# Kernel optimization log

Hardware: AMD Instinct MI355X
Metric: run time of the kernel (lower is better)

The kernel has to match this reference:

```python
import jax, jax.numpy as jnp
import numpy as np

N, E, FS = 50000, 400000, 256
H, D = 8, 64            # GAT heads, hidden_size (per-head out_feats)
NH, DK, DV = 8, 64, 64  # transformer MHA
B = 1024
NEG_SLOPE = 0.2
EPS = 1e-6


def _layer_norm(x, g, b, eps=EPS):
    mu = x.mean(-1, keepdims=True)
    var = x.var(-1, keepdims=True)
    return (x - mu) / jnp.sqrt(var + eps) * g + b


def setup_inputs() -> dict:
    key = jax.random.key(0)
    ks = jax.random.split(key, 20)
    s = 0.02
    return {
        "features": jax.random.normal(ks[0], (N, FS), jnp.float32),
        "src": jax.random.randint(ks[1], (E,), 0, N, jnp.int32),
        "dst": jax.random.randint(ks[2], (E,), 0, N, jnp.int32),
        "url": jax.random.randint(ks[3], (B,), 1, N + 1, jnp.int32),  # 1-based ids
        # GATConv params (DGL-style)
        "gat_fc_w": jax.random.normal(ks[4], (FS, H * D), jnp.float32) * s,
        "attn_l": jax.random.normal(ks[5], (H, D), jnp.float32) * s,
        "attn_r": jax.random.normal(ks[6], (H, D), jnp.float32) * s,
        "gat_res_w": jax.random.normal(ks[7], (FS, H * D), jnp.float32) * s,
        "gat_bias": jnp.zeros((H, D), jnp.float32),
        # post-GAT LayerNorm
        "ln_g": jnp.ones((D,), jnp.float32),
        "ln_b": jnp.zeros((D,), jnp.float32),
        # MultiHeadAttention params
        "wq": jax.random.normal(ks[8], (D, NH * DK), jnp.float32) * s,
        "wk": jax.random.normal(ks[9], (D, NH * DK), jnp.float32) * s,
        "wv": jax.random.normal(ks[10], (D, NH * DV), jnp.float32) * s,
        "fc_w": jax.random.normal(ks[11], (NH * DV, D), jnp.float32) * s,
        "fc_b": jnp.zeros((D,), jnp.float32),
        "mha_ln_g": jnp.ones((D,), jnp.float32),
        "mha_ln_b": jnp.zeros((D,), jnp.float32),
        # final classifier
        "out_w": jax.random.normal(ks[12], (D, 2), jnp.float32) * s,
        "out_b": jnp.zeros((2,), jnp.float32),
    }


def reference(features, src, dst, url, gat_fc_w, attn_l, attn_r, gat_res_w,
              gat_bias, ln_g, ln_b, wq, wk, wv, fc_w, fc_b, mha_ln_g,
              mha_ln_b, out_w, out_b):
    # ---- GATConv (residual=True, bias, negative_slope=0.2, no activation) ----
    feat = (features @ gat_fc_w).reshape(N, H, D)          # [N,H,D]
    el = jnp.einsum('nhd,hd->nh', feat, attn_l)            # [N,H]
    er = jnp.einsum('nhd,hd->nh', feat, attn_r)            # [N,H]
    e = jax.nn.leaky_relu(el[src] + er[dst], NEG_SLOPE)    # [E,H] edge scores
    # segment softmax over incoming edges of each dst node
    m = jax.ops.segment_max(e, dst, num_segments=N)        # [N,H]
    m = jnp.where(jnp.isfinite(m), m, 0.0)
    ex = jnp.exp(e - m[dst])                               # [E,H]
    denom = jax.ops.segment_sum(ex, dst, num_segments=N)   # [N,H]
    a = ex / jnp.maximum(denom[dst], 1e-20)                # [E,H]
    msg = feat[src] * a[:, :, None]                        # [E,H,D]
    rst = jax.ops.segment_sum(msg, dst, num_segments=N)    # [N,H,D]
    res = (features @ gat_res_w).reshape(N, H, D)
    gat_emb = rst + res + gat_bias                         # [N,H,D]

    # ---- select batch nodes (url is 1-based) ----
    ids = url - 1
    x = gat_emb[ids]                                       # [B,H,D]
    x = _layer_norm(x, ln_g, ln_b)

    # ---- dense multi-head self-attention over the H gat heads (seq dim) ----
    residual = x
    q = (x @ wq).reshape(B, H, NH, DK)
    k = (x @ wk).reshape(B, H, NH, DK)
    v = (x @ wv).reshape(B, H, NH, DV)
    attn = jnp.einsum('bqhd,bkhd->bhqk', q, k) / jnp.sqrt(jnp.float32(DK))
    attn = jax.nn.softmax(attn, axis=-1)
    o = jnp.einsum('bhqk,bkhd->bqhd', attn, v).reshape(B, H, NH * DV)
    o = o @ fc_w + fc_b                                    # [B,H,D]
    o = _layer_norm(o + residual, mha_ln_g, mha_ln_b)

    # ---- pool + classify ----
    pooled = o.sum(axis=1)                                 # [B,D]
    logits = pooled @ out_w + out_b                        # [B,2]
    return logits
```

## Files before the change

### kernel.cpp

```cpp
#include <hip/hip_runtime.h>
#include <math.h>

#define Nn 50000
#define Ee 400000
#define FSz 256
#define HD_ 512
#define Bb 1024

static __device__ __forceinline__ int clampi(int v, int lo, int hi){
    return v < lo ? lo : (v > hi ? hi : v);
}
static __device__ __forceinline__ unsigned short f2bf(float f){
    unsigned int u = __float_as_uint(f);
    unsigned int r = u + 0x7FFFu + ((u >> 16) & 1u);
    return (unsigned short)(r >> 16);
}
static __device__ __forceinline__ float bflo(unsigned int v){ return __uint_as_float(v << 16); }
static __device__ __forceinline__ float bfhi(unsigned int v){ return __uint_as_float(v & 0xFFFF0000u); }

__global__ __launch_bounds__(256) void k_mark(const int* __restrict__ url, int* uid, int* unode, int* cnt,
                                              const float* __restrict__ W,
                                              const float* __restrict__ al,
                                              const float* __restrict__ ar,
                                              float* __restrict__ wl, float* __restrict__ wr){
    int t = threadIdx.x;
    if(blockIdx.x >= 4){
        int bi = blockIdx.x - 4;
        int wv = t >> 6, lane = t & 63;
        #pragma unroll
        for(int r = 0; r < 4; r++){
            int f = bi*16 + wv*4 + r;
            float pl[8], pr[8];
            #pragma unroll
            for(int h = 0; h < 8; h++){
                float w = W[f*512 + h*64 + lane];
                pl[h] = w * al[h*64 + lane];
                pr[h] = w * ar[h*64 + lane];
            }
            #pragma unroll
            for(int h = 0; h < 8; h++){
                #pragma unroll
                for(int m = 32; m >= 1; m >>= 1){
                    pl[h] += __shfl_xor(pl[h], m, 64);
                    pr[h] += __shfl_xor(pr[h], m, 64);
                }
            }
            #pragma unroll
            for(int h = 0; h < 8; h++){
                if(lane == h){ wl[h*256 + f] = pl[h]; wr[h*256 + f] = pr[h]; }
            }
        }
    } else {
        int b = blockIdx.x * 256 + t;
        if(b < Bb){
            int n = clampi(url[b] - 1, 0, Nn - 1);
            int old = atomicCAS(&uid[n], -1, -2);
            if(old == -1){
                int id = atomicAdd(cnt, 1);
                unode[id] = n;
                uid[n] = id;
            }
        }
    }
}

__global__ __launch_bounds__(256) void k_scatter(const int* __restrict__ src, const int* __restrict__ dst,
                                                 const int* __restrict__ uid, int* __restrict__ fill,
                                                 int* __restrict__ slist){
    int e = blockIdx.x * 256 + threadIdx.x;
    if(e >= Ee) return;
    int d = dst[e];
    if((unsigned)d >= (unsigned)Nn) return;
    int u = uid[d];
    if(u < 0) return;
    int pos = atomicAdd(&fill[u], 1);
    if(pos >= 64) return;
    slist[u*64 + pos] = clampi(src[e], 0, Nn - 1);
}

__global__ __launch_bounds__(256) void k_gat(const float* __restrict__ features,
                                             const float* __restrict__ Wfc,
                                             const float* __restrict__ Wres,
                                             const float* __restrict__ bias,
                                             const float* __restrict__ wl,
                                             const float* __restrict__ wr,
                                             const int* __restrict__ cnt, const int* __restrict__ unode,
                                             const int* __restrict__ fill, const int* __restrict__ slist,
                                             float* __restrict__ gemb){
    int t = threadIdx.x;
    int lane = t & 63, wv = t >> 6;
    int cntv = cnt[0];
    int u0 = blockIdx.x * 4;
    if(u0 >= cntv) return;

    __shared__ float cxs[4][8][256];
    __shared__ float fres[4][256];
    __shared__ float sew[4][64][8];
    __shared__ float ser[4][8];
    __shared__ int   sslist[4][64];

    for(int i = t; i < 4*64*8; i += 256) ((float*)sew)[i] = 0.f;

    float4 rwl[8], rwr[8];
    #pragma unroll
    for(int h = 0; h < 8; h++){
        rwl[h] = *(const float4*)&wl[h*256 + 4*lane];
        rwr[h] = *(const float4*)&wr[h*256 + 4*lane];
    }

    int dg[4];
    #pragma unroll
    for(int j = 0; j < 4; j++){
        int u = u0 + j;
        dg[j] = (u < cntv) ? min(fill[u], 64) : 0;
        if(t < dg[j]) sslist[j][t] = slist[u*64 + t];
        if(u < cntv) fres[j][t] = features[(size_t)unode[u] * FSz + t];
        else         fres[j][t] = 0.f;
    }
    __syncthreads();

    int c1 = dg[0], c2 = c1 + dg[1], c3 = c2 + dg[2];
    int total = c3 + dg[3];
    for(int tau = wv; tau < total + 4; tau += 4){
        int j, i, isEr = 0;
        if(tau < c1){ j = 0; i = tau; }
        else if(tau < c2){ j = 1; i = tau - c1; }
        else if(tau < c3){ j = 2; i = tau - c2; }
        else if(tau < total){ j = 3; i = tau - c3; }
        else { j = tau - total; i = 0; isEr = 1; }
        int s = isEr ? ((u0 + j < cntv) ? unode[u0 + j] : 0) : sslist[j][i];
        float4 x = *(const float4*)(features + (size_t)s * FSz + 4*lane);
        float p[8];
        if(isEr){
            #pragma unroll
            for(int h = 0; h < 8; h++)
                p[h] = x.x*rwr[h].x + x.y*rwr[h].y + x.z*rwr[h].z + x.w*rwr[h].w;
        } else {
            #pragma unroll
            for(int h = 0; h < 8; h++)
                p[h] = x.x*rwl[h].x + x.y*rwl[h].y + x.z*rwl[h].z + x.w*rwl[h].w;
        }
        #pragma unroll
        for(int h = 0; h < 8; h++){
            #pragma unroll
            for(int m = 32; m >= 1; m >>= 1) p[h] += __shfl_xor(p[h], m, 64);
        }
        if(lane == 0){
            if(isEr){
                #pragma unroll
                for(int h = 0; h < 8; h++) ser[j][h] = p[h];
            } else {
                #pragma unroll
                for(int h = 0; h < 8; h++) sew[j][i][h] = p[h];
            }
        }
    }
    __syncthreads();
    if(t < 32){
        int j = t >> 3, h = t & 7;
        int dgj = dg[j];
        if(dgj > 0){
            float ern = ser[j][h];
            float m = -1e30f;
            for(int i = 0; i < dgj; i++){
                float v = sew[j][i][h] + ern;
                v = v > 0.f ? v : 0.2f * v;
                m = fmaxf(m, v);
            }
            float sum = 0.f;
            for(int i = 0; i < dgj; i++){
                float v = sew[j][i][h] + ern;
                v = v > 0.f ? v : 0.2f * v;
                float w = expf(v - m);
                sum += w;
                sew[j][i][h] = w;
            }
            float inv = 1.0f / fmaxf(sum, 1e-20f);
            for(int i = 0; i < dgj; i++) sew[j][i][h] *= inv;
        }
    }
    __syncthreads();
    {
        float cx[4][8];
        #pragma unroll
        for(int j = 0; j < 4; j++)
            #pragma unroll
            for(int h = 0; h < 8; h++) cx[j][h] = 0.f;
        int mxd = max(max(dg[0], dg[1]), max(dg[2], dg[3]));
        for(int i = 0; i < mxd; i++){
            float x[4];
            #pragma unroll
            for(int j = 0; j < 4; j++){
                int s = (i < dg[j]) ? sslist[j][i] : 0;
                x[j] = features[(size_t)s * FSz + t];
            }
            #pragma unroll
            for(int j = 0; j < 4; j++){
                const float* av = &sew[j][i][0];
                float xm = (i < dg[j]) ? x[j] : 0.f;
                #pragma unroll
                for(int h = 0; h < 8; h++) cx[j][h] += av[h] * xm;
            }
        }
        #pragma unroll
        for(int j = 0; j < 4; j++)
            #pragma unroll
            for(int h = 0; h < 8; h++) cxs[j][h][t] = cx[j][h];
    }
    __syncthreads();

    int h = t >> 5;
    int o0 = 2 * t;
    const float2* Wfc2  = (const float2*)Wfc;
    const float2* Wres2 = (const float2*)Wres;
    float a[4][2] = {{0,0},{0,0},{0,0},{0,0}};
    for(int f = 0; f < 256; f += 4){
        float2 w0 = Wfc2[(f+0)*256 + t];
        float2 w1 = Wfc2[(f+1)*256 + t];
        float2 w2 = Wfc2[(f+2)*256 + t];
        float2 w3 = Wfc2[(f+3)*256 + t];
        float2 r0 = Wres2[(f+0)*256 + t];
        float2 r1 = Wres2[(f+1)*256 + t];
        float2 r2 = Wres2[(f+2)*256 + t];
        float2 r3 = Wres2[(f+3)*256 + t];
        #pragma unroll
        for(int j = 0; j < 4; j++){
            float4 c = *(const float4*)&cxs[j][h][f];
            float4 x = *(const float4*)&fres[j][f];
            a[j][0] += c.x*w0.x + c.y*w1.x + c.z*w2.x + c.w*w3.x
                     + x.x*r0.x + x.y*r1.x + x.z*r2.x + x.w*r3.x;
            a[j][1] += c.x*w0.y + c.y*w1.y + c.z*w2.y + c.w*w3.y
                     + x.x*r0.y + x.y*r1.y + x.z*r2.y + x.w*r3.y;
        }
    }
    float b0 = bias[o0], b1 = bias[o0 + 1];
    #pragma unroll
    for(int j = 0; j < 4; j++){
        if(u0 + j < cntv){
            float2* gp = (float2*)(gemb + (size_t)(u0 + j) * HD_);
            gp[t] = make_float2(a[j][0] + b0, a[j][1] + b1);
        }
    }
}

__global__ __launch_bounds__(256, 4) void k_mha(const int* __restrict__ url, const int* __restrict__ uid,
                                             const float* __restrict__ gemb,
                                             const float* __restrict__ lng, const float* __restrict__ lnb,
                                             const float* __restrict__ wq, const float* __restrict__ wk,
                                             const float* __restrict__ wvp, const float* __restrict__ fcw,
                                             const float* __restrict__ fcb, const float* __restrict__ mlg,
                                             const float* __restrict__ mlb, const float* __restrict__ outw,
                                             const float* __restrict__ outb, float* __restrict__ out){
    __shared__ float A[512];
    __shared__ float xnF[512];
    __shared__ unsigned short xnT[64*8];
    __shared__ unsigned short qkb[2*8*520];
    __shared__ float mu8[8], rs8[8], pooled[64];

    int b = blockIdx.x, t = threadIdx.x;
    int lane = t & 63, wv = t >> 6;
    int n = clampi(url[b] - 1, 0, Nn - 1);
    int u = uid[n];
    if(u < 0) u = 0;
    const float* gp = gemb + (size_t)u * HD_;
    A[t] = gp[t]; A[t + 256] = gp[t + 256];
    __syncthreads();
    if(t < 8){
        float s = 0.f, s2 = 0.f;
        for(int d = 0; d < 64; d++){ float v = A[t*64 + d]; s += v; s2 += v * v; }
        float mu = s * (1.0f/64.0f);
        float var = s2 * (1.0f/64.0f) - mu * mu;
        mu8[t] = mu; rs8[t] = rsqrtf(fmaxf(var, 0.0f) + 1e-6f);
    }
    __syncthreads();
    #pragma unroll
    for(int p = 0; p < 2; p++){
        int i = p*256 + t; int q = i >> 6, d = i & 63;
        float xv = (A[i] - mu8[q]) * rs8[q] * lng[d] + lnb[d];
        xnF[i] = xv;
        xnT[d*8 + q] = f2bf(xv);
    }
    __syncthreads();
    float aq0[8] = {0,0,0,0,0,0,0,0}, aq1[8] = {0,0,0,0,0,0,0,0};
    float ak0[8] = {0,0,0,0,0,0,0,0}, ak1[8] = {0,0,0,0,0,0,0,0};
    float av0[8] = {0,0,0,0,0,0,0,0}, av1[8] = {0,0,0,0,0,0,0,0};
    #pragma unroll 2
    for(int d = 0; d < 64; d++){
        float q0 = wq[d*512 + t],  q1 = wq[d*512 + t + 256];
        float k0 = wk[d*512 + t],  k1 = wk[d*512 + t + 256];
        float v0 = wvp[d*512 + t], v1 = wvp[d*512 + t + 256];
        uint4 xp = *(const uint4*)&xnT[d*8];
        float xv[8] = { bflo(xp.x), bfhi(xp.x), bflo(xp.y), bfhi(xp.y),
                        bflo(xp.z), bfhi(xp.z), bflo(xp.w), bfhi(xp.w) };
        #pragma unroll
        for(int r = 0; r < 8; r++){
            aq0[r] += xv[r]*q0; aq1[r] += xv[r]*q1;
            ak0[r] += xv[r]*k0; ak1[r] += xv[r]*k1;
            av0[r] += xv[r]*v0; av1[r] += xv[r]*v1;
        }
    }
    #pragma unroll
    for(int qq = 0; qq < 8; qq++){
        qkb[qq*520 + t]              = f2bf(aq0[qq]);
        qkb[qq*520 + t + 256]        = f2bf(aq1[qq]);
        qkb[4160 + qq*520 + t]       = f2bf(ak0[qq]);
        qkb[4160 + qq*520 + t + 256] = f2bf(ak1[qq]);
    }
    __syncthreads();
    #pragma unroll
    for(int p = 0; p < 2; p++){
        int idx = p*256 + t;
        int nh = idx >> 6, qq = (idx >> 3) & 7, kk = idx & 7;
        const unsigned short* qrow = &qkb[qq*520 + nh*64];
        const unsigned short* krow = &qkb[4160 + kk*520 + nh*64];
        float s = 0.f;
        #pragma unroll
        for(int d8 = 0; d8 < 64; d8 += 8){
            uint4 qv = *(const uint4*)&qrow[d8];
            uint4 kv = *(const uint4*)&krow[d8];
            s += bflo(qv.x)*bflo(kv.x) + bfhi(qv.x)*bfhi(kv.x)
               + bflo(qv.y)*bflo(kv.y) + bfhi(qv.y)*bfhi(kv.y)
               + bflo(qv.z)*bflo(kv.z) + bfhi(qv.z)*bfhi(kv.z)
               + bflo(qv.w)*bflo(kv.w) + bfhi(qv.w)*bfhi(kv.w);
        }
        A[idx] = s * 0.125f;
    }
    __syncthreads();
    if(t < 64){
        float mx = -1e30f;
        #pragma unroll
        for(int k = 0; k < 8; k++) mx = fmaxf(mx, A[t*8 + k]);
        float e[8]; float s = 0.f;
        #pragma unroll
        for(int k = 0; k < 8; k++){ e[k] = expf(A[t*8 + k] - mx); s += e[k]; }
        float inv = 1.0f / s;
        #pragma unroll
        for(int k = 0; k < 8; k++) A[t*8 + k] = e[k] * inv;
    }
    __syncthreads();
    {
        int nh0 = wv;
        #pragma unroll
        for(int qq = 0; qq < 8; qq++){
            const float* s0 = &A[nh0*64 + qq*8];
            const float* s1 = &A[(nh0+4)*64 + qq*8];
            float4 a0 = *(const float4*)s0, b0 = *(const float4*)(s0 + 4);
            float4 a1 = *(const float4*)s1, b1 = *(const float4*)(s1 + 4);
            float o0 = a0.x*av0[0] + a0.y*av0[1] + a0.z*av0[2] + a0.w*av0[3]
                     + b0.x*av0[4] + b0.y*av0[5] + b0.z*av0[6] + b0.w*av0[7];
            float o1 = a1.x*av1[0] + a1.y*av1[1] + a1.z*av1[2] + a1.w*av1[3]
                     + b1.x*av1[4] + b1.y*av1[5] + b1.z*av1[6] + b1.w*av1[7];
            qkb[qq*520 + t]       = f2bf(o0);
            qkb[qq*520 + t + 256] = f2bf(o1);
        }
    }
    __syncthreads();
    {
        float* P = (float*)&qkb[4160];
        int g = lane & 31;
        int qh = lane >> 5;
        int k0 = wv * 128;
        float a[4][2] = {{0,0},{0,0},{0,0},{0,0}};
        const float2* fw2 = (const float2*)fcw;
        for(int k = k0; k < k0 + 128; k += 8){
            float2 f0 = fw2[(k+0)*32 + g];
            float2 f1 = fw2[(k+1)*32 + g];
            float2 f2 = fw2[(k+2)*32 + g];
            float2 f3 = fw2[(k+3)*32 + g];
            float2 f4 = fw2[(k+4)*32 + g];
            float2 f5 = fw2[(k+5)*32 + g];
            float2 f6 = fw2[(k+6)*32 + g];
            float2 f7 = fw2[(k+7)*32 + g];
            #pragma unroll
            for(int jq = 0; jq < 4; jq++){
                int qq = qh*4 + jq;
                uint4 op = *(const uint4*)&qkb[qq*520 + k];
                float x0 = bflo(op.x), x1 = bfhi(op.x), x2 = bflo(op.y), x3 = bfhi(op.y);
                float x4 = bflo(op.z), x5 = bfhi(op.z), x6 = bflo(op.w), x7 = bfhi(op.w);
                a[jq][0] += x0*f0.x + x1*f1.x + x2*f2.x + x3*f3.x + x4*f4.x + x5*f5.x + x6*f6.x + x7*f7.x;
                a[jq][1] += x0*f0.y + x1*f1.y + x2*f2.y + x3*f3.y + x4*f4.y + x5*f5.y + x6*f6.y + x7*f7.y;
            }
        }
        __syncthreads();
        #pragma unroll
        for(int jq = 0; jq < 4; jq++){
            int qq = qh*4 + jq;
            *(float2*)&P[wv*512 + qq*64 + 2*g] = make_float2(a[jq][0], a[jq][1]);
        }
        __syncthreads();
        #pragma unroll
        for(int p = 0; p < 2; p++){
            int o = p*256 + t;
            int dd = o & 63;
            A[o] = P[o] + P[512 + o] + P[1024 + o] + P[1536 + o] + fcb[dd] + xnF[o];
        }
    }
    __syncthreads();
    if(t < 8){
        float s = 0.f, s2 = 0.f;
        for(int d = 0; d < 64; d++){ float v = A[t*64 + d]; s += v; s2 += v * v; }
        float mu = s * (1.0f/64.0f);
        float var = s2 * (1.0f/64.0f) - mu * mu;
        mu8[t] = mu; rs8[t] = rsqrtf(fmaxf(var, 0.0f) + 1e-6f);
    }
    __syncthreads();
    if(t < 64){
        float g2 = mlg[t], bb = mlb[t];
        float s = 0.f;
        #pragma unroll
        for(int qq = 0; qq < 8; qq++)
            s += (A[qq*64 + t] - mu8[qq]) * rs8[qq] * g2 + bb;
        pooled[t] = s;
    }
    __syncthreads();
    if(t < 2){
        float s = outb[t];
        for(int d = 0; d < 64; d++) s += pooled[d] * outw[d*2 + t];
        out[b*2 + t] = s;
    }
}

extern "C" void kernel_launch(void* const* d_in, const int* in_sizes, int n_in,
                              void* d_out, int out_size, void* d_ws, size_t ws_size,
                              hipStream_t stream){
    (void)in_sizes; (void)n_in; (void)out_size; (void)ws_size;
    const float* features  = (const float*)d_in[0];
    const int*   src       = (const int*)d_in[1];
    const int*   dst       = (const int*)d_in[2];
    const int*   url       = (const int*)d_in[3];
    const float* gat_fc_w  = (const float*)d_in[4];
    const float* attn_l    = (const float*)d_in[5];
    const float* attn_r    = (const float*)d_in[6];
    const float* gat_res_w = (const float*)d_in[7];
    const float* gat_bias  = (const float*)d_in[8];
    const float* ln_g      = (const float*)d_in[9];
    const float* ln_b      = (const float*)d_in[10];
    const float* wq        = (const float*)d_in[11];
    const float* wk        = (const float*)d_in[12];
    const float* wv        = (const float*)d_in[13];
    const float* fc_w      = (const float*)d_in[14];
    const float* fc_b      = (const float*)d_in[15];
    const float* mha_ln_g  = (const float*)d_in[16];
    const float* mha_ln_b  = (const float*)d_in[17];
    const float* out_w     = (const float*)d_in[18];
    const float* out_b     = (const float*)d_in[19];

    char* base = (char*)d_ws;
    size_t cur = 0;
    auto alloc = [&](size_t nbytes) -> void* {
        void* p = base + cur;
        cur = (cur + nbytes + 255) & ~(size_t)255;
        return p;
    };
    float* wl    = (float*)alloc(2048 * sizeof(float));
    float* wr    = (float*)alloc(2048 * sizeof(float));
    int*   uid   = (int*)alloc((size_t)Nn * sizeof(int));
    int*   unode = (int*)alloc(1024 * sizeof(int));
    int*   fill  = (int*)alloc(1056 * sizeof(int));
    int*   cnt   = fill + 1024;
    int*   slist = (int*)alloc((size_t)1024 * 64 * sizeof(int));
    float* gemb  = (float*)alloc((size_t)1024 * 512 * sizeof(float));

    hipMemsetAsync(uid, 0xFF, (size_t)Nn * sizeof(int), stream);
    hipMemsetAsync(fill, 0, 1056 * sizeof(int), stream);

    hipLaunchKernelGGL(k_mark,    dim3(20),   dim3(256), 0, stream, url, uid, unode, cnt,
                       gat_fc_w, attn_l, attn_r, wl, wr);
    hipLaunchKernelGGL(k_scatter, dim3(1563), dim3(256), 0, stream, src, dst, uid, fill, slist);
    hipLaunchKernelGGL(k_gat,     dim3(256),  dim3(256), 0, stream, features, gat_fc_w, gat_res_w, gat_bias,
                       wl, wr, cnt, unode, fill, slist, gemb);
    hipLaunchKernelGGL(k_mha,     dim3(1024), dim3(256), 0, stream, url, uid, gemb, ln_g, ln_b,
                       wq, wk, wv, fc_w, fc_b, mha_ln_g, mha_ln_b, out_w, out_b,
                       (float*)d_out);
}
```

Measured before the change: 220.9 us.

## Replace global node-id map with per-block shared hash; batch two samples per MHA block

The scatter kernel now builds a per-block shared-memory hash table from url to batch indices and scatters each edge to every batch entry that shares the destination node. This removes the 50K-entry uid memset, the separate mark kernel and the dedup step. The GAT kernel now processes all 1024 batch entries directly, duplicates included, so it does redundant work when url repeats. The MHA kernel handles two batch rows per block, reusing each weight load across both, at the cost of more registers and occupancy lowered from 4 to 2.

```diff
diff --git a/kernel.cpp b/kernel.cpp
--- a/kernel.cpp
+++ b/kernel.cpp
@@ -6,6 +6,7 @@
 #define FSz 256
 #define HD_ 512
 #define Bb 1024
+#define HSZ 2048
 
 static __device__ __forceinline__ int clampi(int v, int lo, int hi){
     return v < lo ? lo : (v > hi ? hi : v);
@@ -18,14 +19,16 @@
 static __device__ __forceinline__ float bflo(unsigned int v){ return __uint_as_float(v << 16); }
 static __device__ __forceinline__ float bfhi(unsigned int v){ return __uint_as_float(v & 0xFFFF0000u); }
 
-__global__ __launch_bounds__(256) void k_mark(const int* __restrict__ url, int* uid, int* unode, int* cnt,
-                                              const float* __restrict__ W,
-                                              const float* __restrict__ al,
-                                              const float* __restrict__ ar,
-                                              float* __restrict__ wl, float* __restrict__ wr){
+__global__ __launch_bounds__(256) void k_scatter(const int* __restrict__ src, const int* __restrict__ dst,
+                                                 const int* __restrict__ url,
+                                                 int* __restrict__ fill, int* __restrict__ slist,
+                                                 const float* __restrict__ W,
+                                                 const float* __restrict__ al,
+                                                 const float* __restrict__ ar,
+                                                 float* __restrict__ wl, float* __restrict__ wr){
     int t = threadIdx.x;
-    if(blockIdx.x >= 4){
-        int bi = blockIdx.x - 4;
+    if(blockIdx.x >= 1563){
+        int bi = blockIdx.x - 1563;
         int wv = t >> 6, lane = t & 63;
         #pragma unroll
         for(int r = 0; r < 4; r++){
@@ -50,32 +53,41 @@
                 if(lane == h){ wl[h*256 + f] = pl[h]; wr[h*256 + f] = pr[h]; }
             }
         }
-    } else {
-        int b = blockIdx.x * 256 + t;
-        if(b < Bb){
-            int n = clampi(url[b] - 1, 0, Nn - 1);
-            int old = atomicCAS(&uid[n], -1, -2);
-            if(old == -1){
-                int id = atomicAdd(cnt, 1);
-                unode[id] = n;
-                uid[n] = id;
-            }
-        }
-    }
-}
-
-__global__ __launch_bounds__(256) void k_scatter(const int* __restrict__ src, const int* __restrict__ dst,
-                                                 const int* __restrict__ uid, int* __restrict__ fill,
-                                                 int* __restrict__ slist){
-    int e = blockIdx.x * 256 + threadIdx.x;
+        return;
+    }
+    __shared__ int key[HSZ];
+    __shared__ int chainhead[HSZ];
+    __shared__ short nxt[Bb];
+    for(int i = t; i < HSZ; i += 256){ key[i] = -1; chainhead[i] = -1; }
+    __syncthreads();
+    for(int b = t; b < Bb; b += 256){
+        int n = clampi(url[b] - 1, 0, Nn - 1);
+        int h = n & (HSZ - 1);
+        while(true){
+            int prev = atomicCAS(&key[h], -1, n);
+            if(prev == -1 || prev == n) break;
+            h = (h + 1) & (HSZ - 1);
+        }
+        int old = atomicExch(&chainhead[h], b);
+        nxt[b] = (short)old;
+    }
+    __syncthreads();
+    int e = blockIdx.x * 256 + t;
     if(e >= Ee) return;
     int d = dst[e];
     if((unsigned)d >= (unsigned)Nn) return;
-    int u = uid[d];
-    if(u < 0) return;
-    int pos = atomicAdd(&fill[u], 1);
-    if(pos >= 64) return;
-    slist[u*64 + pos] = clampi(src[e], 0, Nn - 1);
+    int h = d & (HSZ - 1);
+    while(true){
+        int k = key[h];
+        if(k == -1) return;
+        if(k == d) break;
+        h = (h + 1) & (HSZ - 1);
+    }
+    int s = clampi(src[e], 0, Nn - 1);
+    for(int b = chainhead[h]; b != -1; b = nxt[b]){
+        int pos = atomicAdd(&fill[b], 1);
+        if(pos < 64) slist[b*64 + pos] = s;
+    }
 }
 
 __global__ __launch_bounds__(256) void k_gat(const float* __restrict__ features,
@@ -84,14 +96,12 @@
                                              const float* __restrict__ bias,
                                              const float* __restrict__ wl,
                                              const float* __restrict__ wr,
-                                             const int* __restrict__ cnt, const int* __restrict__ unode,
+                                             const int* __restrict__ url,
                                              const int* __restrict__ fill, const int* __restrict__ slist,
                                              float* __restrict__ gemb){
     int t = threadIdx.x;
     int lane = t & 63, wv = t >> 6;
-    int cntv = cnt[0];
     int u0 = blockIdx.x * 4;
-    if(u0 >= cntv) return;
 
     __shared__ float cxs[4][8][256];
     __shared__ float fres[4][256];
@@ -108,14 +118,14 @@
         rwr[h] = *(const float4*)&wr[h*256 + 4*lane];
     }
 
-    int dg[4];
+    int dg[4], nj[4];
     #pragma unroll
     for(int j = 0; j < 4; j++){
         int u = u0 + j;
-        dg[j] = (u < cntv) ? min(fill[u], 64) : 0;
+        dg[j] = min(fill[u], 64);
+        nj[j] = clampi(url[u] - 1, 0, Nn - 1);
         if(t < dg[j]) sslist[j][t] = slist[u*64 + t];
-        if(u < cntv) fres[j][t] = features[(size_t)unode[u] * FSz + t];
-        else         fres[j][t] = 0.f;
+        fres[j][t] = features[(size_t)nj[j] * FSz + t];
     }
     __syncthreads();
 
@@ -128,7 +138,7 @@
         else if(tau < c3){ j = 2; i = tau - c2; }
         else if(tau < total){ j = 3; i = tau - c3; }
         else { j = tau - total; i = 0; isEr = 1; }
-        int s = isEr ? ((u0 + j < cntv) ? unode[u0 + j] : 0) : sslist[j][i];
+        int s = isEr ? nj[j] : sslist[j][i];
         float4 x = *(const float4*)(features + (size_t)s * FSz + 4*lane);
         float p[8];
         if(isEr){
@@ -236,83 +246,95 @@
     float b0 = bias[o0], b1 = bias[o0 + 1];
     #pragma unroll
     for(int j = 0; j < 4; j++){
-        if(u0 + j < cntv){
-            float2* gp = (float2*)(gemb + (size_t)(u0 + j) * HD_);
-            gp[t] = make_float2(a[j][0] + b0, a[j][1] + b1);
-        }
+        float2* gp = (float2*)(gemb + (size_t)(u0 + j) * HD_);
+        gp[t] = make_float2(a[j][0] + b0, a[j][1] + b1);
     }
 }
 
-__global__ __launch_bounds__(256, 4) void k_mha(const int* __restrict__ url, const int* __restrict__ uid,
-                                             const float* __restrict__ gemb,
+__global__ __launch_bounds__(256, 2) void k_mha(const float* __restrict__ gemb,
                                              const float* __restrict__ lng, const float* __restrict__ lnb,
                                              const float* __restrict__ wq, const float* __restrict__ wk,
                                              const float* __restrict__ wvp, const float* __restrict__ fcw,
                                              const float* __restrict__ fcb, const float* __restrict__ mlg,
                                              const float* __restrict__ mlb, const float* __restrict__ outw,
                                              const float* __restrict__ outb, float* __restrict__ out){
-    __shared__ float A[512];
-    __shared__ float xnF[512];
-    __shared__ unsigned short xnT[64*8];
-    __shared__ unsigned short qkb[2*8*520];
-    __shared__ float mu8[8], rs8[8], pooled[64];
-
-    int b = blockIdx.x, t = threadIdx.x;
+    __shared__ float A[2][512];
+    __shared__ float xnF[2][512];
+    __shared__ unsigned short xnT[2][512];
+    __shared__ unsigned short qkb[2][8320];
+    __shared__ float mu8[2][8], rs8[2][8], pooled[2][64];
+
+    int t = threadIdx.x;
     int lane = t & 63, wv = t >> 6;
-    int n = clampi(url[b] - 1, 0, Nn - 1);
-    int u = uid[n];
-    if(u < 0) u = 0;
-    const float* gp = gemb + (size_t)u * HD_;
-    A[t] = gp[t]; A[t + 256] = gp[t + 256];
-    __syncthreads();
-    if(t < 8){
+    int e0 = blockIdx.x * 2;
+
+    {
+        const float* g0 = gemb + (size_t)e0 * HD_;
+        const float* g1 = gemb + (size_t)(e0 + 1) * HD_;
+        A[0][t] = g0[t]; A[0][t + 256] = g0[t + 256];
+        A[1][t] = g1[t]; A[1][t + 256] = g1[t + 256];
+    }
+    __syncthreads();
+    if(t < 16){
+        int ee = t >> 3, q = t & 7;
         float s = 0.f, s2 = 0.f;
-        for(int d = 0; d < 64; d++){ float v = A[t*64 + d]; s += v; s2 += v * v; }
+        for(int d = 0; d < 64; d++){ float v = A[ee][q*64 + d]; s += v; s2 += v * v; }
         float mu = s * (1.0f/64.0f);
         float var = s2 * (1.0f/64.0f) - mu * mu;
-        mu8[t] = mu; rs8[t] = rsqrtf(fmaxf(var, 0.0f) + 1e-6f);
-    }
-    __syncthreads();
-    #pragma unroll
-    for(int p = 0; p < 2; p++){
-        int i = p*256 + t; int q = i >> 6, d = i & 63;
-        float xv = (A[i] - mu8[q]) * rs8[q] * lng[d] + lnb[d];
-        xnF[i] = xv;
-        xnT[d*8 + q] = f2bf(xv);
-    }
-    __syncthreads();
-    float aq0[8] = {0,0,0,0,0,0,0,0}, aq1[8] = {0,0,0,0,0,0,0,0};
-    float ak0[8] = {0,0,0,0,0,0,0,0}, ak1[8] = {0,0,0,0,0,0,0,0};
-    float av0[8] = {0,0,0,0,0,0,0,0}, av1[8] = {0,0,0,0,0,0,0,0};
+        mu8[ee][q] = mu; rs8[ee][q] = rsqrtf(fmaxf(var, 0.0f) + 1e-6f);
+    }
+    __syncthreads();
+    #pragma unroll
+    for(int p = 0; p < 4; p++){
+        int i = p*256 + t; int ee = i >> 9, ii = i & 511, q = ii >> 6, d = ii & 63;
+        float xv = (A[ee][ii] - mu8[ee][q]) * rs8[ee][q] * lng[d] + lnb[d];
+        xnF[ee][ii] = xv;
+        xnT[ee][d*8 + q] = f2bf(xv);
+    }
+    __syncthreads();
+    float aq0[2][8], aq1[2][8], ak0[2][8], ak1[2][8], av0[2][8], av1[2][8];
+    #pragma unroll
+    for(int ee = 0; ee < 2; ee++)
+        #pragma unroll
+        for(int r = 0; r < 8; r++){
+            aq0[ee][r]=0.f; aq1[ee][r]=0.f; ak0[ee][r]=0.f;
+            ak1[ee][r]=0.f; av0[ee][r]=0.f; av1[ee][r]=0.f;
+        }
     #pragma unroll 2
     for(int d = 0; d < 64; d++){
         float q0 = wq[d*512 + t],  q1 = wq[d*512 + t + 256];
         float k0 = wk[d*512 + t],  k1 = wk[d*512 + t + 256];
         float v0 = wvp[d*512 + t], v1 = wvp[d*512 + t + 256];
-        uint4 xp = *(const uint4*)&xnT[d*8];
-        float xv[8] = { bflo(xp.x), bfhi(xp.x), bflo(xp.y), bfhi(xp.y),
-                        bflo(xp.z), bfhi(xp.z), bflo(xp.w), bfhi(xp.w) };
-        #pragma unroll
-        for(int r = 0; r < 8; r++){
-            aq0[r] += xv[r]*q0; aq1[r] += xv[r]*q1;
-            ak0[r] += xv[r]*k0; ak1[r] += xv[r]*k1;
-            av0[r] += xv[r]*v0; av1[r] += xv[r]*v1;
-        }
-    }
-    #pragma unroll
-    for(int qq = 0; qq < 8; qq++){
-        qkb[qq*520 + t]              = f2bf(aq0[qq]);
-        qkb[qq*520 + t + 256]        = f2bf(aq1[qq]);
-        qkb[4160 + qq*520 + t]       = f2bf(ak0[qq]);
-        qkb[4160 + qq*520 + t + 256] = f2bf(ak1[qq]);
-    }
-    __syncthreads();
-    #pragma unroll
-    for(int p = 0; p < 2; p++){
-        int idx = p*256 + t;
+        #pragma unroll
+        for(int ee = 0; ee < 2; ee++){
+            uint4 xp = *(const uint4*)&xnT[ee][d*8];
+            float xv[8] = { bflo(xp.x), bfhi(xp.x), bflo(xp.y), bfhi(xp.y),
+                            bflo(xp.z), bfhi(xp.z), bflo(xp.w), bfhi(xp.w) };
+            #pragma unroll
+            for(int r = 0; r < 8; r++){
+                aq0[ee][r] += xv[r]*q0; aq1[ee][r] += xv[r]*q1;
+                ak0[ee][r] += xv[r]*k0; ak1[ee][r] += xv[r]*k1;
+                av0[ee][r] += xv[r]*v0; av1[ee][r] += xv[r]*v1;
+            }
+        }
+    }
+    #pragma unroll
+    for(int ee = 0; ee < 2; ee++)
+        #pragma unroll
+        for(int qq = 0; qq < 8; qq++){
+            qkb[ee][qq*520 + t]              = f2bf(aq0[ee][qq]);
+            qkb[ee][qq*520 + t + 256]        = f2bf(aq1[ee][qq]);
+            qkb[ee][4160 + qq*520 + t]       = f2bf(ak0[ee][qq]);
+            qkb[ee][4160 + qq*520 + t + 256] = f2bf(ak1[ee][qq]);
+        }
+    __syncthreads();
+    #pragma unroll
+    for(int p = 0; p < 4; p++){
+        int i = p*256 + t;
+        int ee = i >> 9, idx = i & 511;
         int nh = idx >> 6, qq = (idx >> 3) & 7, kk = idx & 7;
-        const unsigned short* qrow = &qkb[qq*520 + nh*64];
-        const unsigned short* krow = &qkb[4160 + kk*520 + nh*64];
+        const unsigned short* qrow = &qkb[ee][qq*520 + nh*64];
+        const unsigned short* krow = &qkb[ee][4160 + kk*520 + nh*64];
         float s = 0.f;
         #pragma unroll
         for(int d8 = 0; d8 < 64; d8 += 8){
@@ -323,46 +345,55 @@
                + bflo(qv.z)*bflo(kv.z) + bfhi(qv.z)*bfhi(kv.z)
                + bflo(qv.w)*bflo(kv.w) + bfhi(qv.w)*bfhi(kv.w);
         }
-        A[idx] = s * 0.125f;
-    }
-    __syncthreads();
-    if(t < 64){
+        A[ee][idx] = s * 0.125f;
+    }
+    __syncthreads();
+    if(t < 128){
+        int ee = t >> 6, row = t & 63;
         float mx = -1e30f;
         #pragma unroll
-        for(int k = 0; k < 8; k++) mx = fmaxf(mx, A[t*8 + k]);
+        for(int k = 0; k < 8; k++) mx = fmaxf(mx, A[ee][row*8 + k]);
         float e[8]; float s = 0.f;
         #pragma unroll
-        for(int k = 0; k < 8; k++){ e[k] = expf(A[t*8 + k] - mx); s += e[k]; }
+        for(int k = 0; k < 8; k++){ e[k] = expf(A[ee][row*8 + k] - mx); s += e[k]; }
         float inv = 1.0f / s;
         #pragma unroll
-        for(int k = 0; k < 8; k++) A[t*8 + k] = e[k] * inv;
+        for(int k = 0; k < 8; k++) A[ee][row*8 + k] = e[k] * inv;
     }
     __syncthreads();
     {
         int nh0 = wv;
         #pragma unroll
-        for(int qq = 0; qq < 8; qq++){
-            const float* s0 = &A[nh0*64 + qq*8];
-            const float* s1 = &A[(nh0+4)*64 + qq*8];
-            float4 a0 = *(const float4*)s0, b0 = *(const float4*)(s0 + 4);
-            float4 a1 = *(const float4*)s1, b1 = *(const float4*)(s1 + 4);
-            float o0 = a0.x*av0[0] + a0.y*av0[1] + a0.z*av0[2] + a0.w*av0[3]
-                     + b0.x*av0[4] + b0.y*av0[5] + b0.z*av0[6] + b0.w*av0[7];
-            float o1 = a1.x*av1[0] + a1.y*av1[1] + a1.z*av1[2] + a1.w*av1[3]
-                     + b1.x*av1[4] + b1.y*av1[5] + b1.z*av1[6] + b1.w*av1[7];
-            qkb[qq*520 + t]       = f2bf(o0);
-            qkb[qq*520 + t + 256] = f2bf(o1);
+        for(int ee = 0; ee < 2; ee++){
+            #pragma unroll
+            for(int qq = 0; qq < 8; qq++){
+                const float* s0 = &A[ee][nh0*64 + qq*8];
+                const float* s1 = &A[ee][(nh0+4)*64 + qq*8];
+                float4 a0 = *(const float4*)s0, b0 = *(const float4*)(s0 + 4);
+                float4 a1 = *(const float4*)s1, b1 = *(const float4*)(s1 + 4);
+                float o0 = a0.x*av0[ee][0] + a0.y*av0[ee][1] + a0.z*av0[ee][2] + a0.w*av0[ee][3]
+                         + b0.x*av0[ee][4] + b0.y*av0[ee][5] + b0.z*av0[ee][6] + b0.w*av0[ee][7];
+                float o1 = a1.x*av1[ee][0] + a1.y*av1[ee][1] + a1.z*av1[ee][2] + a1.w*av1[ee][3]
+                         + b1.x*av1[ee][4] + b1.y*av1[ee][5] + b1.z*av1[ee][6] + b1.w*av1[ee][7];
+                qkb[ee][qq*520 + t]       = f2bf(o0);
+                qkb[ee][qq*520 + t + 256] = f2bf(o1);
+            }
         }
     }
     __syncthreads();
     {
-        float* P = (float*)&qkb[4160];
+        float* P0 = (float*)&qkb[0][4160];
+        float* P1 = (float*)&qkb[1][4160];
         int g = lane & 31;
         int qh = lane >> 5;
-        int k0 = wv * 128;
-        float a[4][2] = {{0,0},{0,0},{0,0},{0,0}};
+        int k0r = wv * 128;
+        float a[2][4][2];
+        #pragma unroll
+        for(int ee = 0; ee < 2; ee++)
+            #pragma unroll
+            for(int jq = 0; jq < 4; jq++){ a[ee][jq][0] = 0.f; a[ee][jq][1] = 0.f; }
         const float2* fw2 = (const float2*)fcw;
-        for(int k = k0; k < k0 + 128; k += 8){
+        for(int k = k0r; k < k0r + 128; k += 8){
             float2 f0 = fw2[(k+0)*32 + g];
             float2 f1 = fw2[(k+1)*32 + g];
             float2 f2 = fw2[(k+2)*32 + g];
@@ -372,51 +403,59 @@
             float2 f6 = fw2[(k+6)*32 + g];
             float2 f7 = fw2[(k+7)*32 + g];
             #pragma unroll
-            for(int jq = 0; jq < 4; jq++){
-                int qq = qh*4 + jq;
-                uint4 op = *(const uint4*)&qkb[qq*520 + k];
-                float x0 = bflo(op.x), x1 = bfhi(op.x), x2 = bflo(op.y), x3 = bfhi(op.y);
-                float x4 = bflo(op.z), x5 = bfhi(op.z), x6 = bflo(op.w), x7 = bfhi(op.w);
-                a[jq][0] += x0*f0.x + x1*f1.x + x2*f2.x + x3*f3.x + x4*f4.x + x5*f5.x + x6*f6.x + x7*f7.x;
-                a[jq][1] += x0*f0.y + x1*f1.y + x2*f2.y + x3*f3.y + x4*f4.y + x5*f5.y + x6*f6.y + x7*f7.y;
+            for(int ee = 0; ee < 2; ee++){
+                #pragma unroll
+                for(int jq = 0; jq < 4; jq++){
+                    int qq = qh*4 + jq;
+                    uint4 op = *(const uint4*)&qkb[ee][qq*520 + k];
+                    float x0 = bflo(op.x), x1 = bfhi(op.x), x2 = bflo(op.y), x3 = bfhi(op.y);
+                    float x4 = bflo(op.z), x5 = bfhi(op.z), x6 = bflo(op.w), x7 = bfhi(op.w);
+                    a[ee][jq][0] += x0*f0.x + x1*f1.x + x2*f2.x + x3*f3.x + x4*f4.x + x5*f5.x + x6*f6.x + x7*f7.x;
+                    a[ee][jq][1] += x0*f0.y + x1*f1.y + x2*f2.y + x3*f3.y + x4*f4.y + x5*f5.y + x6*f6.y + x7*f7.y;
+                }
             }
         }
         __syncthreads();
         #pragma unroll
         for(int jq = 0; jq < 4; jq++){
             int qq = qh*4 + jq;
-            *(float2*)&P[wv*512 + qq*64 + 2*g] = make_float2(a[jq][0], a[jq][1]);
+            *(float2*)&P0[wv*512 + qq*64 + 2*g] = make_float2(a[0][jq][0], a[0][jq][1]);
+            *(float2*)&P1[wv*512 + qq*64 + 2*g] = make_float2(a[1][jq][0], a[1][jq][1]);
         }
         __syncthreads();
         #pragma unroll
-        for(int p = 0; p < 2; p++){
-            int o = p*256 + t;
-            int dd = o & 63;
-            A[o] = P[o] + P[512 + o] + P[1024 + o] + P[1536 + o] + fcb[dd] + xnF[o];
-        }
-    }
-    __syncthreads();
-    if(t < 8){
+        for(int p = 0; p < 4; p++){
+            int i = p*256 + t;
+            int ee = i >> 9, o = i & 511, dd = o & 63;
+            const float* P = ee ? P1 : P0;
+            A[ee][o] = P[o] + P[512 + o] + P[1024 + o] + P[1536 + o] + fcb[dd] + xnF[ee][o];
+        }
+    }
+    __syncthreads();
+    if(t < 16){
+        int ee = t >> 3, q = t & 7;
         float s = 0.f, s2 = 0.f;
-        for(int d = 0; d < 64; d++){ float v = A[t*64 + d]; s += v; s2 += v * v; }
+        for(int d = 0; d < 64; d++){ float v = A[ee][q*64 + d]; s += v; s2 += v * v; }
         float mu = s * (1.0f/64.0f);
         float var = s2 * (1.0f/64.0f) - mu * mu;
-        mu8[t] = mu; rs8[t] = rsqrtf(fmaxf(var, 0.0f) + 1e-6f);
-    }
-    __syncthreads();
-    if(t < 64){
-        float g2 = mlg[t], bb = mlb[t];
+        mu8[ee][q] = mu; rs8[ee][q] = rsqrtf(fmaxf(var, 0.0f) + 1e-6f);
+    }
+    __syncthreads();
+    if(t < 128){
+        int ee = t >> 6, dd = t & 63;
+        float g2 = mlg[dd], bb = mlb[dd];
         float s = 0.f;
         #pragma unroll
         for(int qq = 0; qq < 8; qq++)
-            s += (A[qq*64 + t] - mu8[qq]) * rs8[qq] * g2 + bb;
-        pooled[t] = s;
-    }
-    __syncthreads();
-    if(t < 2){
-        float s = outb[t];
-        for(int d = 0; d < 64; d++) s += pooled[d] * outw[d*2 + t];
-        out[b*2 + t] = s;
+            s += (A[ee][qq*64 + dd] - mu8[ee][qq]) * rs8[ee][qq] * g2 + bb;
+        pooled[ee][dd] = s;
+    }
+    __syncthreads();
+    if(t < 4){
+        int ee = t >> 1, c = t & 1;
+        float s = outb[c];
+        for(int d = 0; d < 64; d++) s += pooled[ee][d] * outw[d*2 + c];
+        out[(e0 + ee)*2 + c] = s;
     }
 }
 
@@ -454,22 +493,17 @@
     };
     float* wl    = (float*)alloc(2048 * sizeof(float));
     float* wr    = (float*)alloc(2048 * sizeof(float));
-    int*   uid   = (int*)alloc((size_t)Nn * sizeof(int));
-    int*   unode = (int*)alloc(1024 * sizeof(int));
-    int*   fill  = (int*)alloc(1056 * sizeof(int));
-    int*   cnt   = fill + 1024;
+    int*   fill  = (int*)alloc(1024 * sizeof(int));
     int*   slist = (int*)alloc((size_t)1024 * 64 * sizeof(int));
     float* gemb  = (float*)alloc((size_t)1024 * 512 * sizeof(float));
 
-    hipMemsetAsync(uid, 0xFF, (size_t)Nn * sizeof(int), stream);
-    hipMemsetAsync(fill, 0, 1056 * sizeof(int), stream);
-
-    hipLaunchKernelGGL(k_mark,    dim3(20),   dim3(256), 0, stream, url, uid, unode, cnt,
+    hipMemsetAsync(fill, 0, 1024 * sizeof(int), stream);
+
+    hipLaunchKernelGGL(k_scatter, dim3(1579), dim3(256), 0, stream, src, dst, url, fill, slist,
                        gat_fc_w, attn_l, attn_r, wl, wr);
-    hipLaunchKernelGGL(k_scatter, dim3(1563), dim3(256), 0, stream, src, dst, uid, fill, slist);
     hipLaunchKernelGGL(k_gat,     dim3(256),  dim3(256), 0, stream, features, gat_fc_w, gat_res_w, gat_bias,
-                       wl, wr, cnt, unode, fill, slist, gemb);
-    hipLaunchKernelGGL(k_mha,     dim3(1024), dim3(256), 0, stream, url, uid, gemb, ln_g, ln_b,
+                       wl, wr, url, fill, slist, gemb);
+    hipLaunchKernelGGL(k_mha,     dim3(512),  dim3(256), 0, stream, gemb, ln_g, ln_b,
                        wq, wk, wv, fc_w, fc_b, mha_ln_g, mha_ln_b, out_w, out_b,
                        (float*)d_out);
 }
```

After: 210.7 us. 4.6% less time.
